# Kernel tuning notes

Measured on AMD Instinct MI355X. Metric: run time of the kernel, lower is better.

## Reference

```python
import jax, jax.numpy as jnp
from jax import lax
import numpy as np

B, N, C_IN, C_OUT, D = 4, 8192, 64, 128, 3
RATIO, RADIUS, MAX_NBR = 0.25, 0.4, 64
S = int(N * RATIO)


def setup_inputs() -> dict:
    key = jax.random.key(0)
    ks = jax.random.split(key, 8)
    h = 64
    d_in = D + C_IN  # PointNetConv message dim: concat([x_j, pos_j - pos_i])
    sc = lambda f: 1.0 / np.sqrt(f)
    return {
        "x": jax.random.normal(ks[0], (B, N, C_IN), jnp.float32),
        "pos": jax.random.normal(ks[1], (B, N, D), jnp.float32),
        "W1": jax.random.normal(ks[2], (d_in, h), jnp.float32) * sc(d_in),
        "b1": jnp.zeros((h,), jnp.float32),
        "W2": jax.random.normal(ks[3], (h, h), jnp.float32) * sc(h),
        "b2": jnp.zeros((h,), jnp.float32),
        "W3": jax.random.normal(ks[4], (h, C_OUT), jnp.float32) * sc(h),
        "b3": jnp.zeros((C_OUT,), jnp.float32),
    }


def fps(pos, n_samples):
    """Farthest point sampling per cloud. pos: [B,N,3] -> idx [B,S] (int32).
    Deterministic start at index 0 (PyG uses random_start; math is identical)."""
    b, n, _ = pos.shape
    start = jnp.zeros((b,), jnp.int32)
    mind = jnp.full((b, n), jnp.inf, pos.dtype)

    def step(carry, _):
        d, last = carry
        p = jnp.take_along_axis(pos, last[:, None, None], axis=1)  # [B,1,3]
        dist = jnp.sum((pos - p) ** 2, axis=-1)  # [B,N]
        d = jnp.minimum(d, dist)
        nxt = jnp.argmax(d, axis=1).astype(jnp.int32)
        return (d, nxt), last

    _, idxs = lax.scan(step, (mind, start), None, length=n_samples)
    return idxs.T  # [B,S]


def radius_neighbors(pos, pos_s, r, k):
    """For each sampled point pick up to k nearest points within radius r.
    Returns nbr_idx [B,S,k] int32 and valid mask [B,S,k] bool."""
    d2 = jnp.sum((pos_s[:, :, None, :] - pos[:, None, :, :]) ** 2, axis=-1)  # [B,S,N]
    score = jnp.where(d2 <= r * r, -d2, -jnp.inf)
    vals, idx = lax.top_k(score, k)  # nearest-first within the ball
    return idx.astype(jnp.int32), vals > -jnp.inf


def gather(a, idx):
    # a: [B,N,C], idx: [B,S,K] -> [B,S,K,C]
    b, s, k = idx.shape
    flat = jnp.take_along_axis(a, idx.reshape(b, s * k, 1), axis=1)
    return flat.reshape(b, s, k, a.shape[-1])


def reference(x, pos, W1, b1, W2, b2, W3, b3):
    fps_idx = fps(pos, S)                                  # [B,S]
    pos_s = jnp.take_along_axis(pos, fps_idx[..., None], axis=1)  # [B,S,3]
    nbr_idx, valid = radius_neighbors(pos, pos_s, RADIUS, MAX_NBR)

    x_n = gather(x, nbr_idx)                               # [B,S,K,C_IN]
    rel = gather(pos, nbr_idx) - pos_s[:, :, None, :]      # [B,S,K,3]
    feat = jnp.concatenate([x_n, rel], axis=-1)            # [B,S,K,C_IN+3]

    h = jax.nn.relu(feat @ W1 + b1)
    h = jax.nn.relu(h @ W2 + b2)
    h = h @ W3 + b3                                        # [B,S,K,C_OUT]

    h = jnp.where(valid[..., None], h, -jnp.inf)
    out = jnp.max(h, axis=2)                               # max aggregation
    any_valid = jnp.any(valid, axis=-1)[..., None]
    out = jnp.where(any_valid, out, 0.0)                   # empty hood -> 0 (scatter_max fill)
    return out, pos_s
```

## Files before the change

### kernel.cpp

```cpp
#include <hip/hip_runtime.h>

#define NB 4
#define NPTS 8192
#define CIN 64
#define COUT 128
#define NS 2048
#define KNBR 64

#define TFPS 1024
#define PPT 8
#define NWAVE 16

#define NCONS 252
#define NWCONS (NCONS * 16)

__device__ __forceinline__ unsigned spread3(unsigned v) {
    v &= 0x3FFu;
    v = (v * 0x00010001u) & 0xFF0000FFu;
    v = (v * 0x00000101u) & 0x0F00F00Fu;
    v = (v * 0x00000011u) & 0xC30C30C3u;
    v = (v * 0x00000005u) & 0x49249249u;
    return v;
}

__device__ __forceinline__ unsigned quant6(float v) {
    float q = fminf(fmaxf((v + 5.0f) * 6.4f, 0.0f), 63.0f);
    return (unsigned)(int)q;
}

#define DPP_UMAX(v, ctrl)                                                     \
    {                                                                         \
        unsigned _t = (unsigned)__builtin_amdgcn_update_dpp(                  \
            (int)(v), (int)(v), (ctrl), 0xF, 0xF, false);                     \
        (v) = ((v) > _t) ? (v) : _t;                                          \
    }

#define DPP_FMAX(v, ctrl)                                                     \
    {                                                                         \
        float _t = __builtin_bit_cast(float, __builtin_amdgcn_update_dpp(     \
            __builtin_bit_cast(int, (v)), __builtin_bit_cast(int, (v)),       \
            (ctrl), 0xF, 0xF, false));                                        \
        (v) = fmaxf((v), _t);                                                 \
    }

#define WSYNC() asm volatile("s_waitcnt lgkmcnt(0)" ::: "memory")

__global__ __launch_bounds__(1024) void mega_kernel(
    const float* __restrict__ pos, const float* __restrict__ x,
    const float* __restrict__ W1, const float* __restrict__ b1,
    const float* __restrict__ W2, const float* __restrict__ b2,
    const float* __restrict__ W3, const float* __restrict__ b3,
    float* __restrict__ out, float* __restrict__ pos_s,
    unsigned long long* __restrict__ pub)
{
    __shared__ __align__(16) char smem[131200];

    const int tid  = threadIdx.x;
    const int lane = tid & 63;
    const int wv   = tid >> 6;
    const int bid  = blockIdx.x;

    if (bid < NB) {
        float* spos = (float*)smem;
        unsigned* skey = (unsigned*)(smem + 98304);
        unsigned long long (*gslot4)[4] =
            (unsigned long long (*)[4])(smem + 131072);

        const int b = bid;
        const float* pb = pos + (size_t)b * NPTS * 3;

        for (int i = tid; i < NPTS * 3; i += TFPS) spos[i] = pb[i];
        __syncthreads();

        for (int i = tid; i < NPTS; i += TFPS) {
            unsigned qx = quant6(spos[i * 3 + 0]);
            unsigned qy = quant6(spos[i * 3 + 1]);
            unsigned qz = quant6(spos[i * 3 + 2]);
            unsigned m  = spread3(qx) | (spread3(qy) << 1) | (spread3(qz) << 2);
            skey[i] = (m << 13) | (unsigned)i;
        }
        __syncthreads();

        for (int k2 = 2; k2 <= NPTS; k2 <<= 1) {
            for (int j = k2 >> 1; j > 0; j >>= 1) {
#pragma unroll
                for (int t = 0; t < NPTS / TFPS; ++t) {
                    int i = tid + t * TFPS, ixj = i ^ j;
                    if (ixj > i) {
                        unsigned a = skey[i], c = skey[ixj];
                        bool up = ((i & k2) == 0);
                        if ((a > c) == up) { skey[i] = c; skey[ixj] = a; }
                    }
                }
                __syncthreads();
            }
        }

        float px[PPT], py[PPT], pz[PPT], md[PPT];
        unsigned oi[PPT];
        float mnx =  __builtin_inff(), mny =  __builtin_inff(), mnz =  __builtin_inff();
        float mxx = -__builtin_inff(), mxy = -__builtin_inff(), mxz = -__builtin_inff();
#pragma unroll
        for (int j = 0; j < PPT; ++j) {
            int o = (int)(skey[tid * PPT + j] & 8191u);
            oi[j] = 8191u - (unsigned)o;
            float xx = spos[o * 3 + 0], yy = spos[o * 3 + 1], zz = spos[o * 3 + 2];
            px[j] = xx; py[j] = yy; pz[j] = zz;
            md[j] = __builtin_inff();
            mnx = fminf(mnx, xx); mxx = fmaxf(mxx, xx);
            mny = fminf(mny, yy); mxy = fmaxf(mxy, yy);
            mnz = fminf(mnz, zz); mxz = fmaxf(mxz, zz);
        }

        if (tid < 16) ((unsigned long long*)(smem + 131072))[tid] = 0ULL;
        if (tid == 0) {
            float c0 = spos[0], c1 = spos[1], c2 = spos[2];
            pos_s[((size_t)b * NS) * 3 + 0] = c0;
            pos_s[((size_t)b * NS) * 3 + 1] = c1;
            pos_s[((size_t)b * NS) * 3 + 2] = c2;
            const unsigned grow = (unsigned)(b * NS);
            const unsigned long long tg =
                ((unsigned long long)(0xA5000000u | grow)) << 32;
            __hip_atomic_store(pub + (size_t)grow * 3 + 0, tg | __float_as_uint(c0),
                               __ATOMIC_RELAXED, __HIP_MEMORY_SCOPE_AGENT);
            __hip_atomic_store(pub + (size_t)grow * 3 + 1, tg | __float_as_uint(c1),
                               __ATOMIC_RELAXED, __HIP_MEMORY_SCOPE_AGENT);
            __hip_atomic_store(pub + (size_t)grow * 3 + 2, tg | __float_as_uint(c2),
                               __ATOMIC_RELAXED, __HIP_MEMORY_SCOPE_AGENT);
        }
        __syncthreads();

        float cx = spos[0], cy = spos[1], cz = spos[2];
        unsigned long long kb = (unsigned long long)0x7F800000u << 32;
        unsigned long long ckey = 0;
        float thr = __builtin_inff();

        for (int s = 1; s < NS; ++s) {
            float lbx = fmaxf(fmaxf(__fsub_rn(mnx, cx), __fsub_rn(cx, mxx)), 0.0f);
            float lby = fmaxf(fmaxf(__fsub_rn(mny, cy), __fsub_rn(cy, mxy)), 0.0f);
            float lbz = fmaxf(fmaxf(__fsub_rn(mnz, cz), __fsub_rn(cz, mxz)), 0.0f);
            float lb2 = lbx * lbx + lby * lby + lbz * lbz;
            bool need = (lb2 < thr);

            if (__any(need)) {
                kb = 0;
#pragma unroll
                for (int j = 0; j < PPT; ++j) {
                    float dx = __fsub_rn(px[j], cx);
                    float dy = __fsub_rn(py[j], cy);
                    float dz = __fsub_rn(pz[j], cz);
                    float d  = __fadd_rn(__fadd_rn(__fmul_rn(dx, dx), __fmul_rn(dy, dy)),
                                         __fmul_rn(dz, dz));
                    float m  = fminf(md[j], d);
                    md[j] = m;
                    unsigned long long kj =
                        ((unsigned long long)__float_as_uint(m) << 32) | oi[j];
                    if (kj > kb) kb = kj;
                }
                thr = __uint_as_float((unsigned)(kb >> 32)) * 1.0011f;

                unsigned vb = (unsigned)(kb >> 32), sb = (unsigned)kb;
                unsigned v = vb;
                DPP_UMAX(v, 0x111); DPP_UMAX(v, 0x112); DPP_UMAX(v, 0x114);
                DPP_UMAX(v, 0x118); DPP_UMAX(v, 0x142); DPP_UMAX(v, 0x143);
                unsigned vwav = (unsigned)__builtin_amdgcn_readlane((int)v, 63);
                unsigned long long tied = __ballot(vb == vwav);
                unsigned swav;
                if (tied & (tied - 1)) {
                    unsigned sc = (vb == vwav) ? sb : 0u;
                    DPP_UMAX(sc, 0x111); DPP_UMAX(sc, 0x112); DPP_UMAX(sc, 0x114);
                    DPP_UMAX(sc, 0x118); DPP_UMAX(sc, 0x142); DPP_UMAX(sc, 0x143);
                    swav = (unsigned)__builtin_amdgcn_readlane((int)sc, 63);
                } else {
                    int wl = (int)__ffsll((unsigned long long)tied) - 1;
                    swav = (unsigned)__builtin_amdgcn_readlane((int)sb, wl);
                }
                ckey = ((unsigned long long)vwav << 32) | swav;
                if (lane == 0) atomicMax(&gslot4[s & 3][wv & 3], ckey);
            } else {
                if (lane == 0) atomicMax(&gslot4[s & 3][wv & 3], ckey);
            }
            if (tid < 4) gslot4[(s + 2) & 3][tid] = 0ULL;
            __syncthreads();

            unsigned long long g0 = gslot4[s & 3][0];
            unsigned long long g1 = gslot4[s & 3][1];
            unsigned long long g2 = gslot4[s & 3][2];
            unsigned long long g3 = gslot4[s & 3][3];
            unsigned long long ga = (g1 > g0) ? g1 : g0;
            unsigned long long gb = (g3 > g2) ? g3 : g2;
            unsigned long long g  = (gb > ga) ? gb : ga;
            int fi = 8191 - (int)((unsigned)g & 8191u);

            cx = spos[fi * 3 + 0];
            cy = spos[fi * 3 + 1];
            cz = spos[fi * 3 + 2];
            if (tid == 0) {
                pos_s[((size_t)b * NS + s) * 3 + 0] = cx;
                pos_s[((size_t)b * NS + s) * 3 + 1] = cy;
                pos_s[((size_t)b * NS + s) * 3 + 2] = cz;
                const unsigned grow = (unsigned)(b * NS + s);
                const unsigned long long tg =
                    ((unsigned long long)(0xA5000000u | grow)) << 32;
                __hip_atomic_store(pub + (size_t)grow * 3 + 0, tg | __float_as_uint(cx),
                                   __ATOMIC_RELAXED, __HIP_MEMORY_SCOPE_AGENT);
                __hip_atomic_store(pub + (size_t)grow * 3 + 1, tg | __float_as_uint(cy),
                                   __ATOMIC_RELAXED, __HIP_MEMORY_SCOPE_AGENT);
                __hip_atomic_store(pub + (size_t)grow * 3 + 2, tg | __float_as_uint(cz),
                                   __ATOMIC_RELAXED, __HIP_MEMORY_SCOPE_AGENT);
            }
        }
    } else {
        unsigned long long* wk = (unsigned long long*)smem + (size_t)wv * 1024;
        const int g = (bid - NB) * 16 + wv;

        int rows[3]; int nr = 0;
        for (int r = g; r < NB * NS; r += NWCONS) rows[nr++] = r;
        if (nr >= 2 && (rows[1] & 2047) < (rows[0] & 2047)) {
            int t = rows[0]; rows[0] = rows[1]; rows[1] = t;
        }
        if (nr == 3) {
            if ((rows[2] & 2047) < (rows[1] & 2047)) {
                int t = rows[1]; rows[1] = rows[2]; rows[2] = t;
                if ((rows[1] & 2047) < (rows[0] & 2047)) {
                    t = rows[0]; rows[0] = rows[1]; rows[1] = t;
                }
            }
        }

        for (int it = 0; it < nr; ++it) {
            const int row = rows[it];
            const int b   = row >> 11;
            const unsigned tagw = 0xA5000000u | (unsigned)row;
            const unsigned long long* pr = pub + (size_t)row * 3;

            float cx, cy, cz;
            int tries = 0;
            for (;;) {
                unsigned long long w0 = __hip_atomic_load(
                    pr + 0, __ATOMIC_RELAXED, __HIP_MEMORY_SCOPE_AGENT);
                unsigned long long w1 = __hip_atomic_load(
                    pr + 1, __ATOMIC_RELAXED, __HIP_MEMORY_SCOPE_AGENT);
                unsigned long long w2 = __hip_atomic_load(
                    pr + 2, __ATOMIC_RELAXED, __HIP_MEMORY_SCOPE_AGENT);
                if ((unsigned)(w0 >> 32) == tagw && (unsigned)(w1 >> 32) == tagw &&
                    (unsigned)(w2 >> 32) == tagw) {
                    cx = __uint_as_float((unsigned)w0);
                    cy = __uint_as_float((unsigned)w1);
                    cz = __uint_as_float((unsigned)w2);
                    break;
                }
                int naps = 1 + tries; if (naps > 32) naps = 32; ++tries;
                for (int z = 0; z < naps; ++z) __builtin_amdgcn_s_sleep(64);
            }

            const float* pb = pos + (size_t)b * NPTS * 3;
            const float R2 = (float)(0.4 * 0.4);

            unsigned cbase = 0;
            for (int t = 0; t < NPTS / 64; ++t) {
                int i = t * 64 + lane;
                float dx = __fsub_rn(pb[i * 3 + 0], cx);
                float dy = __fsub_rn(pb[i * 3 + 1], cy);
                float dz = __fsub_rn(pb[i * 3 + 2], cz);
                float d2 = __fadd_rn(__fadd_rn(__fmul_rn(dx, dx), __fmul_rn(dy, dy)),
                                     __fmul_rn(dz, dz));
                bool in = (d2 <= R2);
                unsigned long long mk = __ballot(in);
                if (in) {
                    unsigned mb = __builtin_amdgcn_mbcnt_hi(
                        (unsigned)(mk >> 32),
                        __builtin_amdgcn_mbcnt_lo((unsigned)mk, 0u));
                    unsigned p = cbase + mb;
                    if (p < 1024u)
                        wk[p] = ((unsigned long long)__float_as_uint(d2) << 32) |
                                (unsigned)i;
                }
                cbase += (unsigned)__popcll(mk);
            }
            int cnt = (int)(cbase < 1024u ? cbase : 1024u);
            WSYNC();

            if (cnt > KNBR) {
                int sz = 128; while (sz < cnt) sz <<= 1;
                for (int i = cnt + lane; i < sz; i += 64) wk[i] = ~0ULL;
                WSYNC();
                for (int k2 = 2; k2 <= sz; k2 <<= 1) {
                    for (int j = k2 >> 1; j > 0; j >>= 1) {
                        for (int t = 0; t < (sz >> 6); ++t) {
                            int i = t * 64 + lane, ixj = i ^ j;
                            if (ixj > i) {
                                unsigned long long a = wk[i], c2 = wk[ixj];
                                bool up = ((i & k2) == 0);
                                if ((a > c2) == up) { wk[i] = c2; wk[ixj] = a; }
                            }
                        }
                        WSYNC();
                    }
                }
            }

            const int kn   = (cnt < KNBR) ? cnt : KNBR;
            const int slot = (lane < kn) ? lane : 0;
            const int idx  = (int)(unsigned)(wk[slot] & 0xffffffffu);

            const float* xr = x + ((size_t)b * NPTS + idx) * CIN;
            float h1[64];
#pragma unroll
            for (int o = 0; o < 64; ++o) h1[o] = b1[o];
#pragma unroll
            for (int t = 0; t < 16; ++t) {
                float4 v = *reinterpret_cast<const float4*>(xr + t * 4);
                float f0 = v.x, f1 = v.y, f2 = v.z, f3 = v.w;
#pragma unroll
                for (int o = 0; o < 64; ++o) h1[o] = fmaf(f0, W1[(t * 4 + 0) * 64 + o], h1[o]);
#pragma unroll
                for (int o = 0; o < 64; ++o) h1[o] = fmaf(f1, W1[(t * 4 + 1) * 64 + o], h1[o]);
#pragma unroll
                for (int o = 0; o < 64; ++o) h1[o] = fmaf(f2, W1[(t * 4 + 2) * 64 + o], h1[o]);
#pragma unroll
                for (int o = 0; o < 64; ++o) h1[o] = fmaf(f3, W1[(t * 4 + 3) * 64 + o], h1[o]);
            }
            {
                float r0 = pb[idx * 3 + 0] - cx;
                float r1 = pb[idx * 3 + 1] - cy;
                float r2 = pb[idx * 3 + 2] - cz;
#pragma unroll
                for (int o = 0; o < 64; ++o) h1[o] = fmaf(r0, W1[64 * 64 + o], h1[o]);
#pragma unroll
                for (int o = 0; o < 64; ++o) h1[o] = fmaf(r1, W1[65 * 64 + o], h1[o]);
#pragma unroll
                for (int o = 0; o < 64; ++o) h1[o] = fmaf(r2, W1[66 * 64 + o], h1[o]);
            }
#pragma unroll
            for (int o = 0; o < 64; ++o) h1[o] = fmaxf(h1[o], 0.0f);

            float h2[64];
#pragma unroll
            for (int o = 0; o < 64; ++o) h2[o] = b2[o];
#pragma unroll
            for (int k = 0; k < 64; ++k) {
                float f = h1[k];
#pragma unroll
                for (int o = 0; o < 64; ++o) h2[o] = fmaf(f, W2[k * 64 + o], h2[o]);
            }
#pragma unroll
            for (int o = 0; o < 64; ++o) h2[o] = fmaxf(h2[o], 0.0f);

            const bool valid = (lane < kn);
            float* orow = out + (size_t)row * COUT;
#pragma unroll
            for (int c = 0; c < 4; ++c) {
                float acc[32];
#pragma unroll
                for (int o = 0; o < 32; ++o) acc[o] = b3[c * 32 + o];
#pragma unroll
                for (int k = 0; k < 64; ++k) {
                    float f = h2[k];
#pragma unroll
                    for (int o = 0; o < 32; ++o)
                        acc[o] = fmaf(f, W3[k * 128 + c * 32 + o], acc[o]);
                }
#pragma unroll
                for (int o = 0; o < 32; ++o) {
                    float v = valid ? acc[o] : -__builtin_inff();
                    DPP_FMAX(v, 0x111); DPP_FMAX(v, 0x112); DPP_FMAX(v, 0x114);
                    DPP_FMAX(v, 0x118); DPP_FMAX(v, 0x142); DPP_FMAX(v, 0x143);
                    acc[o] = v;
                }
                if (lane == 63) {
#pragma unroll
                    for (int q = 0; q < 8; ++q) {
                        float4 v;
                        v.x = acc[q * 4 + 0]; v.y = acc[q * 4 + 1];
                        v.z = acc[q * 4 + 2]; v.w = acc[q * 4 + 3];
                        *reinterpret_cast<float4*>(orow + c * 32 + q * 4) = v;
                    }
                }
            }
        }
    }
}

extern "C" void kernel_launch(void* const* d_in, const int* in_sizes, int n_in,
                              void* d_out, int out_size, void* d_ws, size_t ws_size,
                              hipStream_t stream)
{
    const float* x   = (const float*)d_in[0];
    const float* pos = (const float*)d_in[1];
    const float* W1  = (const float*)d_in[2];
    const float* b1  = (const float*)d_in[3];
    const float* W2  = (const float*)d_in[4];
    const float* b2  = (const float*)d_in[5];
    const float* W3  = (const float*)d_in[6];
    const float* b3  = (const float*)d_in[7];

    float* out   = (float*)d_out;
    float* pos_s = out + (size_t)NB * NS * COUT;
    unsigned long long* pub = (unsigned long long*)d_ws;

    mega_kernel<<<dim3(NB + NCONS), dim3(1024), 0, stream>>>(
        pos, x, W1, b1, W2, b2, W3, b3, out, pos_s, pub);
}
```

Before: 1.545 ms.

## Shrink FPS block to 512 threads with split float max and interleaved consumer rows

The farthest-point-sampling block now runs 512 threads holding 16 points each, so each per-step cross-wave reduction involves 8 waves and two atomic slots instead of 16 waves and four. The per-thread argmax becomes two independent float-max chains followed by a separate index pass, replacing the serial 64-bit key compare. Consumer blocks also shrink to 8 waves and take rows interleaved across the four clouds in sample order, replacing the sorted per-wave row lists. The aim is to shorten the serial FPS critical path, at the cost of more work per FPS thread and half as many consumer waves in flight.

After: 1.825 ms. +18.1%, slower.

```diff
diff --git a/kernel.cpp b/kernel.cpp
--- a/kernel.cpp
+++ b/kernel.cpp
@@ -7,12 +7,12 @@
 #define NS 2048
 #define KNBR 64
 
-#define TFPS 1024
-#define PPT 8
-#define NWAVE 16
+#define TFPS 512
+#define PPT 16
+#define NWAVE 8
 
 #define NCONS 252
-#define NWCONS (NCONS * 16)
+#define NWCONS (NCONS * 8)
 
 __device__ __forceinline__ unsigned spread3(unsigned v) {
     v &= 0x3FFu;
@@ -45,7 +45,7 @@
 
 #define WSYNC() asm volatile("s_waitcnt lgkmcnt(0)" ::: "memory")
 
-__global__ __launch_bounds__(1024) void mega_kernel(
+__global__ __launch_bounds__(512) void mega_kernel(
     const float* __restrict__ pos, const float* __restrict__ x,
     const float* __restrict__ W1, const float* __restrict__ b1,
     const float* __restrict__ W2, const float* __restrict__ b2,
@@ -63,8 +63,8 @@
     if (bid < NB) {
         float* spos = (float*)smem;
         unsigned* skey = (unsigned*)(smem + 98304);
-        unsigned long long (*gslot4)[4] =
-            (unsigned long long (*)[4])(smem + 131072);
+        unsigned long long (*gslot)[2] =
+            (unsigned long long (*)[2])(smem + 131072);
 
         const int b = bid;
         const float* pb = pos + (size_t)b * NPTS * 3;
@@ -112,7 +112,7 @@
             mnz = fminf(mnz, zz); mxz = fmaxf(mxz, zz);
         }
 
-        if (tid < 16) ((unsigned long long*)(smem + 131072))[tid] = 0ULL;
+        if (tid < 8) ((unsigned long long*)(smem + 131072))[tid] = 0ULL;
         if (tid == 0) {
             float c0 = spos[0], c1 = spos[1], c2 = spos[2];
             pos_s[((size_t)b * NS) * 3 + 0] = c0;
@@ -131,7 +131,6 @@
         __syncthreads();
 
         float cx = spos[0], cy = spos[1], cz = spos[2];
-        unsigned long long kb = (unsigned long long)0x7F800000u << 32;
         unsigned long long ckey = 0;
         float thr = __builtin_inff();
 
@@ -143,23 +142,36 @@
             bool need = (lb2 < thr);
 
             if (__any(need)) {
-                kb = 0;
-#pragma unroll
-                for (int j = 0; j < PPT; ++j) {
-                    float dx = __fsub_rn(px[j], cx);
-                    float dy = __fsub_rn(py[j], cy);
-                    float dz = __fsub_rn(pz[j], cz);
-                    float d  = __fadd_rn(__fadd_rn(__fmul_rn(dx, dx), __fmul_rn(dy, dy)),
-                                         __fmul_rn(dz, dz));
-                    float m  = fminf(md[j], d);
-                    md[j] = m;
-                    unsigned long long kj =
-                        ((unsigned long long)__float_as_uint(m) << 32) | oi[j];
-                    if (kj > kb) kb = kj;
-                }
-                thr = __uint_as_float((unsigned)(kb >> 32)) * 1.0011f;
-
-                unsigned vb = (unsigned)(kb >> 32), sb = (unsigned)kb;
+                float mv0 = 0.0f, mv1 = 0.0f;
+#pragma unroll
+                for (int j = 0; j < PPT / 2; ++j) {
+                    float dx0 = __fsub_rn(px[j], cx);
+                    float dy0 = __fsub_rn(py[j], cy);
+                    float dz0 = __fsub_rn(pz[j], cz);
+                    float d0  = __fadd_rn(__fadd_rn(__fmul_rn(dx0, dx0),
+                                                    __fmul_rn(dy0, dy0)),
+                                          __fmul_rn(dz0, dz0));
+                    float m0  = fminf(md[j], d0);
+                    md[j] = m0; mv0 = fmaxf(mv0, m0);
+
+                    float dx1 = __fsub_rn(px[j + PPT / 2], cx);
+                    float dy1 = __fsub_rn(py[j + PPT / 2], cy);
+                    float dz1 = __fsub_rn(pz[j + PPT / 2], cz);
+                    float d1  = __fadd_rn(__fadd_rn(__fmul_rn(dx1, dx1),
+                                                    __fmul_rn(dy1, dy1)),
+                                          __fmul_rn(dz1, dz1));
+                    float m1  = fminf(md[j + PPT / 2], d1);
+                    md[j + PPT / 2] = m1; mv1 = fmaxf(mv1, m1);
+                }
+                float mv = fmaxf(mv0, mv1);
+                thr = mv * 1.0011f;
+
+                unsigned sb = 0;
+#pragma unroll
+                for (int j = 0; j < PPT; ++j)
+                    if (md[j] == mv && oi[j] > sb) sb = oi[j];
+
+                unsigned vb = __float_as_uint(mv);
                 unsigned v = vb;
                 DPP_UMAX(v, 0x111); DPP_UMAX(v, 0x112); DPP_UMAX(v, 0x114);
                 DPP_UMAX(v, 0x118); DPP_UMAX(v, 0x142); DPP_UMAX(v, 0x143);
@@ -176,20 +188,16 @@
                     swav = (unsigned)__builtin_amdgcn_readlane((int)sb, wl);
                 }
                 ckey = ((unsigned long long)vwav << 32) | swav;
-                if (lane == 0) atomicMax(&gslot4[s & 3][wv & 3], ckey);
+                if (lane == 0) atomicMax(&gslot[s & 3][wv & 1], ckey);
             } else {
-                if (lane == 0) atomicMax(&gslot4[s & 3][wv & 3], ckey);
-            }
-            if (tid < 4) gslot4[(s + 2) & 3][tid] = 0ULL;
+                if (lane == 0) atomicMax(&gslot[s & 3][wv & 1], ckey);
+            }
+            if (tid < 2) gslot[(s + 2) & 3][tid] = 0ULL;
             __syncthreads();
 
-            unsigned long long g0 = gslot4[s & 3][0];
-            unsigned long long g1 = gslot4[s & 3][1];
-            unsigned long long g2 = gslot4[s & 3][2];
-            unsigned long long g3 = gslot4[s & 3][3];
-            unsigned long long ga = (g1 > g0) ? g1 : g0;
-            unsigned long long gb = (g3 > g2) ? g3 : g2;
-            unsigned long long g  = (gb > ga) ? gb : ga;
+            unsigned long long g0 = gslot[s & 3][0];
+            unsigned long long g1 = gslot[s & 3][1];
+            unsigned long long g  = (g1 > g0) ? g1 : g0;
             int fi = 8191 - (int)((unsigned)g & 8191u);
 
             cx = spos[fi * 3 + 0];
@@ -212,25 +220,12 @@
         }
     } else {
         unsigned long long* wk = (unsigned long long*)smem + (size_t)wv * 1024;
-        const int g = (bid - NB) * 16 + wv;
-
-        int rows[3]; int nr = 0;
-        for (int r = g; r < NB * NS; r += NWCONS) rows[nr++] = r;
-        if (nr >= 2 && (rows[1] & 2047) < (rows[0] & 2047)) {
-            int t = rows[0]; rows[0] = rows[1]; rows[1] = t;
-        }
-        if (nr == 3) {
-            if ((rows[2] & 2047) < (rows[1] & 2047)) {
-                int t = rows[1]; rows[1] = rows[2]; rows[2] = t;
-                if ((rows[1] & 2047) < (rows[0] & 2047)) {
-                    t = rows[0]; rows[0] = rows[1]; rows[1] = t;
-                }
-            }
-        }
-
-        for (int it = 0; it < nr; ++it) {
-            const int row = rows[it];
-            const int b   = row >> 11;
+        const int g = (bid - NB) * 8 + wv;
+
+        for (int m = g; m < NB * NS; m += NWCONS) {
+            const int b    = m & 3;
+            const int srow = m >> 2;
+            const int row  = b * NS + srow;
             const unsigned tagw = 0xA5000000u | (unsigned)row;
             const unsigned long long* pr = pub + (size_t)row * 3;
 
@@ -399,6 +394,6 @@
     float* pos_s = out + (size_t)NB * NS * COUT;
     unsigned long long* pub = (unsigned long long*)d_ws;
 
-    mega_kernel<<<dim3(NB + NCONS), dim3(1024), 0, stream>>>(
+    mega_kernel<<<dim3(NB + NCONS), dim3(TFPS), 0, stream>>>(
         pos, x, W1, b1, W2, b2, W3, b3, out, pos_s, pub);
 }
```
